# Performance work log

Measured on AMD Instinct MI355X. Metric: run time of the kernel, lower is better.

## Reference

```python
import jax, jax.numpy as jnp
import numpy as np

D_MODEL = 2048
N_HEADS = 16
D_HEAD = D_MODEL // N_HEADS  # 128
WINDOW = 512
SCALE = D_HEAD ** -0.5


def setup_inputs() -> dict:
    key = jax.random.key(0)
    ks = jax.random.split(key, 5)
    B, S = 2, 4096
    x = jax.random.normal(ks[0], (B, S, D_MODEL), dtype=jnp.float32)
    W_qkv = jax.random.normal(ks[1], (D_MODEL, 3 * D_MODEL), dtype=jnp.float32) * (D_MODEL ** -0.5)
    b_qkv = jax.random.normal(ks[2], (3 * D_MODEL,), dtype=jnp.float32) * 0.02
    W_out = jax.random.normal(ks[3], (D_MODEL, D_MODEL), dtype=jnp.float32) * (D_MODEL ** -0.5)
    b_out = jax.random.normal(ks[4], (D_MODEL,), dtype=jnp.float32) * 0.02
    return {"x": x, "W_qkv": W_qkv, "b_qkv": b_qkv, "W_out": W_out, "b_out": b_out}


def reference(x, W_qkv, b_qkv, W_out, b_out):
    B, S, D = x.shape
    nb = S // WINDOW  # number of independent causal windows (block-diagonal attention)
    qkv = x @ W_qkv + b_qkv  # (B,S,3D)
    q, k, v = jnp.split(qkv, 3, axis=-1)

    def to_blocks(t):
        # (B,S,D) -> (B,H,nb,W,dh)
        return t.reshape(B, nb, WINDOW, N_HEADS, D_HEAD).transpose(0, 3, 1, 2, 4)

    q, k, v = to_blocks(q), to_blocks(k), to_blocks(v)
    # per-window attention scores: (B,H,nb,W,W)
    scores = jnp.einsum('bhnqd,bhnkd->bhnqk', q, k) * SCALE
    causal = jnp.tril(jnp.ones((WINDOW, WINDOW), dtype=bool))
    scores = jnp.where(causal, scores, -jnp.inf)
    attn = jax.nn.softmax(scores, axis=-1)
    out = jnp.einsum('bhnqk,bhnkd->bhnqd', attn, v)  # (B,H,nb,W,dh)
    out = out.transpose(0, 2, 3, 1, 4).reshape(B, S, D)
    return out @ W_out + b_out
```

## Files before the change

### kernel.cpp

```cpp
#include <hip/hip_runtime.h>
#include <stdint.h>


typedef unsigned short u16;
typedef unsigned int u32;
typedef __attribute__((ext_vector_type(8))) short bf16x8;
typedef __attribute__((ext_vector_type(4))) float f32x4;

#define QKVN 6144
#define DM 2048

__device__ __forceinline__ u16 f2b(float f) {
  u32 u = __builtin_bit_cast(u32, f);
  u32 r = (u + 0x7fffu + ((u >> 16) & 1u)) >> 16;
  return (u16)r;
}

__device__ __forceinline__ void gload_lds16(const void* g, void* l) {
  __builtin_amdgcn_global_load_lds((const __attribute__((address_space(1))) void*)g,
                                   (__attribute__((address_space(3))) void*)l,
                                   16, 0, 0);
}


__global__ void cast_f32_bf16(const float4* __restrict__ x, uint4* __restrict__ o) {
  int idx = blockIdx.x * 256 + threadIdx.x;
  float4 a = x[2 * idx];
  float4 b = x[2 * idx + 1];
  uint4 r;
  r.x = (u32)f2b(a.x) | ((u32)f2b(a.y) << 16);
  r.y = (u32)f2b(a.z) | ((u32)f2b(a.w) << 16);
  r.z = (u32)f2b(b.x) | ((u32)f2b(b.y) << 16);
  r.w = (u32)f2b(b.z) | ((u32)f2b(b.w) << 16);
  o[idx] = r;
}

__global__ void transpose_cast(const float* __restrict__ W, u16* __restrict__ Wt,
                               int K, int N) {
  __shared__ u16 tile[64][65];
  int tx = threadIdx.x & 63;
  int ty = threadIdx.x >> 6;
  int n0 = blockIdx.x * 64;
  int k0 = blockIdx.y * 64;
#pragma unroll
  for (int r = 0; r < 64; r += 4)
    tile[r + ty][tx] = f2b(W[(size_t)(k0 + r + ty) * N + n0 + tx]);
  __syncthreads();
#pragma unroll
  for (int r = 0; r < 64; r += 4)
    Wt[(size_t)(n0 + r + ty) * K + k0 + tx] = tile[tx][r + ty];
}


template <typename TO>
__global__ __launch_bounds__(256, 3) void gemm_bt(const u16* __restrict__ A,
                                                  const u16* __restrict__ Bt,
                                                  const float* __restrict__ bias,
                                                  TO* __restrict__ C,
                                                  int M, int N, int K) {
  __shared__ u16 As[128 * 64];
  __shared__ u16 Bs[128 * 64];
  const int tid = threadIdx.x;
  const int lane = tid & 63;
  const int wave = tid >> 6;
  const int quad = lane >> 4;
  const int l15 = lane & 15;
  const int m0 = blockIdx.y * 128;
  const int n0 = blockIdx.x * 128;
  const int wm = (wave & 1) * 64;
  const int wn = (wave >> 1) * 64;

  f32x4 acc[4][4] = {};

  for (int k0 = 0; k0 < K; k0 += 64) {
#pragma unroll
    for (int i = 0; i < 4; ++i) {
      int sb = wave * 256 + i * 64;
      int s = sb + lane;
      int m = s >> 3;
      int c = (s & 7) ^ (m & 7);
      gload_lds16(A + (size_t)(m0 + m) * K + (k0 + c * 8), As + sb * 8);
      gload_lds16(Bt + (size_t)(n0 + m) * K + (k0 + c * 8), Bs + sb * 8);
    }
    __syncthreads();
#pragma unroll
    for (int ks = 0; ks < 2; ++ks) {
      bf16x8 af[4], bf[4];
#pragma unroll
      for (int i = 0; i < 4; ++i) {
        int m = wm + i * 16 + l15;
        af[i] = *(const bf16x8*)(As + m * 64 + (((ks * 4 + quad) ^ (m & 7)) << 3));
        int n = wn + i * 16 + l15;
        bf[i] = *(const bf16x8*)(Bs + n * 64 + (((ks * 4 + quad) ^ (n & 7)) << 3));
      }
#pragma unroll
      for (int i = 0; i < 4; ++i)
#pragma unroll
        for (int j = 0; j < 4; ++j)
          acc[i][j] = __builtin_amdgcn_mfma_f32_16x16x32_bf16(af[i], bf[j], acc[i][j], 0, 0, 0);
    }
    __syncthreads();
  }

#pragma unroll
  for (int j = 0; j < 4; ++j) {
    int col = n0 + wn + j * 16 + l15;
    float bv = bias[col];
#pragma unroll
    for (int i = 0; i < 4; ++i) {
      int row = m0 + wm + i * 16 + quad * 4;
#pragma unroll
      for (int t = 0; t < 4; ++t) {
        float v = acc[i][j][t] + bv;
        if constexpr (sizeof(TO) == 2)
          C[(size_t)(row + t) * N + col] = (TO)f2b(v);
        else
          C[(size_t)(row + t) * N + col] = (TO)v;
      }
    }
  }
}


__global__ __launch_bounds__(256, 2) void attn_win(const u16* __restrict__ qkv,
                                                   u16* __restrict__ attn_out) {
  __shared__ u16 Vt[128 * 64];
  __shared__ u16 Ps[128 * 64];
  const int tid = threadIdx.x;
  const int lane = tid & 63;
  const int wave = tid >> 6;
  const int quad = lane >> 4;
  const int l15 = lane & 15;
  const int qt = blockIdx.x;
  const int win = blockIdx.y;
  const int b = blockIdx.z >> 4;
  const int h = blockIdx.z & 15;
  const int tokw = b * 4096 + win * 512;
  const int tokq = tokw + qt * 128;
  const float SCALE = 0.08838834764831845f;

  bf16x8 qf[2][4];
  {
    const u16* Qb = qkv + (size_t)tokq * QKVN + h * 128;
#pragma unroll
    for (int j = 0; j < 2; ++j) {
      const u16* Qr = Qb + (size_t)(wave * 32 + j * 16 + l15) * QKVN + quad * 8;
#pragma unroll
      for (int ks = 0; ks < 4; ++ks)
        qf[j][ks] = *(const bf16x8*)(Qr + ks * 32);
    }
  }

  f32x4 acc_o[8][2] = {};
  float mrun[2] = {-1e30f, -1e30f};
  float lrun[2] = {0.f, 0.f};

  const int jt_end = 2 * qt + 1;
  for (int jt = 0; jt <= jt_end; ++jt) {
    {
      const u16* Vb = qkv + (size_t)(tokw + jt * 64) * QKVN + 4096 + h * 128;
#pragma unroll
      for (int it = 0; it < 2; ++it) {
        int task = it * 256 + tid;
        int p = task & 31;
        int dc = task >> 5;
        int kk0 = p * 2;
        const u16* g0 = Vb + (size_t)kk0 * QKVN + dc * 8;
        uint4 r0 = *(const uint4*)g0;
        uint4 r1 = *(const uint4*)(g0 + QKVN);
        const u16* a0 = (const u16*)&r0;
        const u16* a1 = (const u16*)&r1;
        int c = kk0 >> 3;
        int boff = (kk0 & 7) << 1;
#pragma unroll
        for (int j = 0; j < 8; ++j) {
          int d = dc * 8 + j;
          *(u32*)((char*)Vt + d * 128 + ((c ^ (d & 7)) << 4) + boff) =
              (u32)a0[j] | ((u32)a1[j] << 16);
        }
      }
    }

    f32x4 acc_s[4][2] = {};
    {
      const u16* Kb = qkv + (size_t)(tokw + jt * 64) * QKVN + 2048 + h * 128;
      bf16x8 kf[4][4];
#pragma unroll
      for (int i = 0; i < 4; ++i) {
        const u16* Kr = Kb + (size_t)(i * 16 + l15) * QKVN + quad * 8;
#pragma unroll
        for (int ks = 0; ks < 4; ++ks)
          kf[i][ks] = *(const bf16x8*)(Kr + ks * 32);
      }
#pragma unroll
      for (int ks = 0; ks < 4; ++ks)
#pragma unroll
        for (int i = 0; i < 4; ++i)
#pragma unroll
          for (int j = 0; j < 2; ++j)
            acc_s[i][j] = __builtin_amdgcn_mfma_f32_16x16x32_bf16(kf[i][ks], qf[j][ks],
                                                                  acc_s[i][j], 0, 0, 0);
    }

    const bool need_mask = (jt >= 2 * qt);
#pragma unroll
    for (int j = 0; j < 2; ++j) {
      int ql = wave * 32 + j * 16 + l15;
      int qg = qt * 128 + ql;
      float vmax = -1e30f;
#pragma unroll
      for (int i = 0; i < 4; ++i)
#pragma unroll
        for (int t = 0; t < 4; ++t) {
          float s = acc_s[i][j][t] * SCALE;
          if (need_mask) {
            int kg = jt * 64 + i * 16 + quad * 4 + t;
            if (kg > qg) s = -1e30f;
          }
          acc_s[i][j][t] = s;
          vmax = fmaxf(vmax, s);
        }
      vmax = fmaxf(vmax, __shfl_xor(vmax, 16));
      vmax = fmaxf(vmax, __shfl_xor(vmax, 32));
      float mnew = fmaxf(mrun[j], vmax);
      float alpha = __expf(mrun[j] - mnew);
      mrun[j] = mnew;
      float vsum = 0.f;
#pragma unroll
      for (int i = 0; i < 4; ++i) {
        float p0 = __expf(acc_s[i][j][0] - mnew);
        float p1 = __expf(acc_s[i][j][1] - mnew);
        float p2 = __expf(acc_s[i][j][2] - mnew);
        float p3 = __expf(acc_s[i][j][3] - mnew);
        vsum += (p0 + p1) + (p2 + p3);
        uint2 pk;
        pk.x = (u32)f2b(p0) | ((u32)f2b(p1) << 16);
        pk.y = (u32)f2b(p2) | ((u32)f2b(p3) << 16);
        int kk = i * 16 + quad * 4;
        *(uint2*)((char*)Ps + ql * 128 + (((kk >> 3) ^ (ql & 7)) << 4) + ((kk & 7) << 1)) = pk;
      }
      vsum += __shfl_xor(vsum, 16);
      vsum += __shfl_xor(vsum, 32);
      lrun[j] = lrun[j] * alpha + vsum;
#pragma unroll
      for (int i2 = 0; i2 < 8; ++i2)
#pragma unroll
        for (int t = 0; t < 4; ++t)
          acc_o[i2][j][t] *= alpha;
    }
    __syncthreads();

#pragma unroll
    for (int ks = 0; ks < 2; ++ks) {
      int kk = ks * 32 + quad * 8;
      int kc = kk >> 3;
      bf16x8 pf[2];
#pragma unroll
      for (int j = 0; j < 2; ++j) {
        int ql = wave * 32 + j * 16 + l15;
        pf[j] = *(const bf16x8*)((char*)Ps + ql * 128 + ((kc ^ (ql & 7)) << 4));
      }
#pragma unroll
      for (int i2 = 0; i2 < 8; ++i2) {
        int d = i2 * 16 + l15;
        bf16x8 vf = *(const bf16x8*)((char*)Vt + d * 128 + ((kc ^ (d & 7)) << 4));
#pragma unroll
        for (int j = 0; j < 2; ++j)
          acc_o[i2][j] = __builtin_amdgcn_mfma_f32_16x16x32_bf16(vf, pf[j], acc_o[i2][j], 0, 0, 0);
      }
    }
    __syncthreads();
  }

#pragma unroll
  for (int j = 0; j < 2; ++j) {
    float inv = 1.0f / lrun[j];
    int ql = wave * 32 + j * 16 + l15;
    u16* orow = attn_out + (size_t)(tokq + ql) * DM + h * 128;
#pragma unroll
    for (int i2 = 0; i2 < 8; ++i2) {
      int d = i2 * 16 + quad * 4;
      uint2 pk;
      pk.x = (u32)f2b(acc_o[i2][j][0] * inv) | ((u32)f2b(acc_o[i2][j][1] * inv) << 16);
      pk.y = (u32)f2b(acc_o[i2][j][2] * inv) | ((u32)f2b(acc_o[i2][j][3] * inv) << 16);
      *(uint2*)(orow + d) = pk;
    }
  }
}


extern "C" void kernel_launch(void* const* d_in, const int* in_sizes, int n_in,
                              void* d_out, int out_size, void* d_ws, size_t ws_size,
                              hipStream_t stream) {
  const float* x = (const float*)d_in[0];
  const float* W_qkv = (const float*)d_in[1];
  const float* b_qkv = (const float*)d_in[2];
  const float* W_out = (const float*)d_in[3];
  const float* b_out = (const float*)d_in[4];
  float* out = (float*)d_out;

  char* w = (char*)d_ws;
  u16* xb = (u16*)w;
  u16* wqkvT = (u16*)(w + 33554432);
  u16* woutT = (u16*)(w + 33554432 + 25165824);
  u16* qkv = (u16*)(w + 67108864);

  cast_f32_bf16<<<8192, 256, 0, stream>>>((const float4*)x, (uint4*)xb);
  transpose_cast<<<dim3(96, 32), 256, 0, stream>>>(W_qkv, wqkvT, 2048, 6144);
  transpose_cast<<<dim3(32, 32), 256, 0, stream>>>(W_out, woutT, 2048, 2048);
  gemm_bt<u16><<<dim3(48, 64), 256, 0, stream>>>(xb, wqkvT, b_qkv, qkv, 8192, 6144, 2048);
  attn_win<<<dim3(4, 8, 32), 256, 0, stream>>>(qkv, xb);
  gemm_bt<float><<<dim3(16, 64), 256, 0, stream>>>(xb, woutT, b_out, out, 8192, 2048, 2048);
}
```

Measured before the change: 522.3 us.

## Replace 128x128 GEMM with 256x256 multi-stage pipelined 8-wave GEMM

Both projection GEMMs now use a 256x256 tile with 8 waves and a 5/4-slot LDS ring buffer. The K loop is split into half-tile phases that interleave asynchronous global-to-LDS loads with MFMA bursts, using explicit waitcnt, barriers and setprio. A grid swizzle improves L2 reuse. It aims to raise arithmetic intensity and hide load latency, at the cost of heavy LDS use (72KB), more registers and fragile hand-tuned synchronization.

```diff
diff --git a/kernel.cpp b/kernel.cpp
--- a/kernel.cpp
+++ b/kernel.cpp
@@ -53,69 +53,167 @@
 
 
 template <typename TO>
-__global__ __launch_bounds__(256, 3) void gemm_bt(const u16* __restrict__ A,
-                                                  const u16* __restrict__ Bt,
-                                                  const float* __restrict__ bias,
-                                                  TO* __restrict__ C,
-                                                  int M, int N, int K) {
-  __shared__ u16 As[128 * 64];
-  __shared__ u16 Bs[128 * 64];
+__global__ __launch_bounds__(512, 2) void gemm_bt256(const u16* __restrict__ A,
+                                                     const u16* __restrict__ Bt,
+                                                     const float* __restrict__ bias,
+                                                     TO* __restrict__ C,
+                                                     int M, int N, int K, int nbx) {
+  __shared__ u16 As[5 * 8192];
+  __shared__ u16 Bs[4 * 8192];
   const int tid = threadIdx.x;
   const int lane = tid & 63;
   const int wave = tid >> 6;
+  const int wr = wave >> 2;
+  const int wc = wave & 3;
   const int quad = lane >> 4;
   const int l15 = lane & 15;
-  const int m0 = blockIdx.y * 128;
-  const int n0 = blockIdx.x * 128;
-  const int wm = (wave & 1) * 64;
-  const int wn = (wave >> 1) * 64;
-
-  f32x4 acc[4][4] = {};
-
-  for (int k0 = 0; k0 < K; k0 += 64) {
-#pragma unroll
-    for (int i = 0; i < 4; ++i) {
-      int sb = wave * 256 + i * 64;
-      int s = sb + lane;
-      int m = s >> 3;
-      int c = (s & 7) ^ (m & 7);
-      gload_lds16(A + (size_t)(m0 + m) * K + (k0 + c * 8), As + sb * 8);
-      gload_lds16(Bt + (size_t)(n0 + m) * K + (k0 + c * 8), Bs + sb * 8);
-    }
-    __syncthreads();
-#pragma unroll
-    for (int ks = 0; ks < 2; ++ks) {
-      bf16x8 af[4], bf[4];
-#pragma unroll
-      for (int i = 0; i < 4; ++i) {
-        int m = wm + i * 16 + l15;
-        af[i] = *(const bf16x8*)(As + m * 64 + (((ks * 4 + quad) ^ (m & 7)) << 3));
-        int n = wn + i * 16 + l15;
-        bf[i] = *(const bf16x8*)(Bs + n * 64 + (((ks * 4 + quad) ^ (n & 7)) << 3));
-      }
-#pragma unroll
-      for (int i = 0; i < 4; ++i)
-#pragma unroll
-        for (int j = 0; j < 4; ++j)
-          acc[i][j] = __builtin_amdgcn_mfma_f32_16x16x32_bf16(af[i], bf[j], acc[i][j], 0, 0, 0);
-    }
-    __syncthreads();
+
+  const int nwg = gridDim.x;
+  const int id = blockIdx.x;
+  const int swz = (id & 7) * (nwg >> 3) + (id >> 3);
+  const int bx = swz % nbx;
+  const int by = swz / nbx;
+  const int m0 = by * 256;
+  const int n0 = bx * 256;
+  const int NT = K >> 6;
+  const int NH = 2 * NT;
+
+  auto stageA = [&](int h, int slot) {
+    if (h < NH) {
+      const u16* src = A + (size_t)(m0 + ((h & 1) << 7)) * K + ((h >> 1) << 6);
+      u16* dst = As + slot * 8192 + (wave << 9);
+#pragma unroll
+      for (int it = 0; it < 2; ++it) {
+        int s = (it << 9) + (wave << 6) + lane;
+        int row = s >> 3;
+        int c = (s & 7) ^ (row & 7);
+        gload_lds16(src + (size_t)row * K + (c << 3), dst + (it << 12));
+      }
+    }
+  };
+  auto stageB = [&](int h, int slot) {
+    if (h < NH) {
+      const u16* src = Bt + (size_t)(n0 + ((h & 1) << 7)) * K + ((h >> 1) << 6);
+      u16* dst = Bs + slot * 8192 + (wave << 9);
+#pragma unroll
+      for (int it = 0; it < 2; ++it) {
+        int s = (it << 9) + (wave << 6) + lane;
+        int row = s >> 3;
+        int c = (s & 7) ^ (row & 7);
+        gload_lds16(src + (size_t)row * K + (c << 3), dst + (it << 12));
+      }
+    }
+  };
+
+  f32x4 acc[8][4] = {};
+  const int axq = l15 & 7;
+  const int aro = l15 << 6;
+  const int c0 = (quad ^ axq) << 3;
+  const int c1 = ((4 + quad) ^ axq) << 3;
+
+  stageA(0, 0); stageB(0, 0);
+  stageA(1, 1); stageB(1, 1);
+  stageA(2, 2); stageB(2, 2);
+  asm volatile("s_waitcnt vmcnt(4)" ::: "memory");
+  __builtin_amdgcn_s_barrier();
+
+  int sa = wr;
+  int h3a = 3;
+  int h4a = 4;
+
+  for (int t = 0; t < NT; ++t) {
+    const u16* ar = As + sa * 8192 + aro;
+    const u16* bp = Bs + (((2 * t + (wc >> 1)) & 3) * 8192) + ((wc & 1) << 12) + aro;
+    bf16x8 a0[4], a1[4], b0[4];
+
+#pragma unroll
+    for (int j = 0; j < 4; ++j) b0[j] = *(const bf16x8*)(bp + j * 1024 + c0);
+#pragma unroll
+    for (int i = 0; i < 4; ++i) a0[i] = *(const bf16x8*)(ar + i * 1024 + c0);
+    stageA(2 * t + 3, h3a);
+    __builtin_amdgcn_s_barrier();
+    asm volatile("s_waitcnt lgkmcnt(0)" ::: "memory");
+    __builtin_amdgcn_sched_barrier(0);
+    __builtin_amdgcn_s_setprio(1);
+#pragma unroll
+    for (int i = 0; i < 4; ++i)
+#pragma unroll
+      for (int j = 0; j < 4; ++j)
+        acc[i][j] = __builtin_amdgcn_mfma_f32_16x16x32_bf16(a0[i], b0[j], acc[i][j], 0, 0, 0);
+    __builtin_amdgcn_s_setprio(0);
+    __builtin_amdgcn_s_barrier();
+
+#pragma unroll
+    for (int i = 0; i < 4; ++i) a1[i] = *(const bf16x8*)(ar + (i + 4) * 1024 + c0);
+    stageB(2 * t + 3, (2 * t + 3) & 3);
+    __builtin_amdgcn_s_barrier();
+    asm volatile("s_waitcnt lgkmcnt(0)" ::: "memory");
+    __builtin_amdgcn_sched_barrier(0);
+    __builtin_amdgcn_s_setprio(1);
+#pragma unroll
+    for (int i = 0; i < 4; ++i)
+#pragma unroll
+      for (int j = 0; j < 4; ++j)
+        acc[i + 4][j] = __builtin_amdgcn_mfma_f32_16x16x32_bf16(a1[i], b0[j], acc[i + 4][j], 0, 0, 0);
+    __builtin_amdgcn_s_setprio(0);
+    __builtin_amdgcn_s_barrier();
+
+#pragma unroll
+    for (int j = 0; j < 4; ++j) b0[j] = *(const bf16x8*)(bp + j * 1024 + c1);
+#pragma unroll
+    for (int i = 0; i < 4; ++i) a0[i] = *(const bf16x8*)(ar + i * 1024 + c1);
+    stageA(2 * t + 4, h4a);
+    __builtin_amdgcn_s_barrier();
+    asm volatile("s_waitcnt lgkmcnt(0)" ::: "memory");
+    __builtin_amdgcn_sched_barrier(0);
+    __builtin_amdgcn_s_setprio(1);
+#pragma unroll
+    for (int i = 0; i < 4; ++i)
+#pragma unroll
+      for (int j = 0; j < 4; ++j)
+        acc[i][j] = __builtin_amdgcn_mfma_f32_16x16x32_bf16(a0[i], b0[j], acc[i][j], 0, 0, 0);
+    __builtin_amdgcn_s_setprio(0);
+    __builtin_amdgcn_s_barrier();
+
+#pragma unroll
+    for (int i = 0; i < 4; ++i) a1[i] = *(const bf16x8*)(ar + (i + 4) * 1024 + c1);
+    stageB(2 * t + 4, (2 * t + 4) & 3);
+    if (t + 3 <= NT) {
+      asm volatile("s_waitcnt vmcnt(4)" ::: "memory");
+    } else if (t + 2 == NT) {
+      asm volatile("s_waitcnt vmcnt(0)" ::: "memory");
+    }
+    __builtin_amdgcn_s_barrier();
+    asm volatile("s_waitcnt lgkmcnt(0)" ::: "memory");
+    __builtin_amdgcn_sched_barrier(0);
+    __builtin_amdgcn_s_setprio(1);
+#pragma unroll
+    for (int i = 0; i < 4; ++i)
+#pragma unroll
+      for (int j = 0; j < 4; ++j)
+        acc[i + 4][j] = __builtin_amdgcn_mfma_f32_16x16x32_bf16(a1[i], b0[j], acc[i + 4][j], 0, 0, 0);
+    __builtin_amdgcn_s_setprio(0);
+    __builtin_amdgcn_s_barrier();
+
+    sa += 2; if (sa >= 5) sa -= 5;
+    h3a += 2; if (h3a >= 5) h3a -= 5;
+    h4a += 2; if (h4a >= 5) h4a -= 5;
   }
 
 #pragma unroll
   for (int j = 0; j < 4; ++j) {
-    int col = n0 + wn + j * 16 + l15;
+    int col = n0 + wc * 64 + j * 16 + l15;
     float bv = bias[col];
 #pragma unroll
-    for (int i = 0; i < 4; ++i) {
-      int row = m0 + wm + i * 16 + quad * 4;
-#pragma unroll
-      for (int t = 0; t < 4; ++t) {
-        float v = acc[i][j][t] + bv;
+    for (int i = 0; i < 8; ++i) {
+      int row = m0 + wr * 128 + i * 16 + quad * 4;
+#pragma unroll
+      for (int tt = 0; tt < 4; ++tt) {
+        float v = acc[i][j][tt] + bv;
         if constexpr (sizeof(TO) == 2)
-          C[(size_t)(row + t) * N + col] = (TO)f2b(v);
+          C[(size_t)(row + tt) * N + col] = (TO)f2b(v);
         else
-          C[(size_t)(row + t) * N + col] = (TO)v;
+          C[(size_t)(row + tt) * N + col] = (TO)v;
       }
     }
   }
@@ -308,7 +406,7 @@
   cast_f32_bf16<<<8192, 256, 0, stream>>>((const float4*)x, (uint4*)xb);
   transpose_cast<<<dim3(96, 32), 256, 0, stream>>>(W_qkv, wqkvT, 2048, 6144);
   transpose_cast<<<dim3(32, 32), 256, 0, stream>>>(W_out, woutT, 2048, 2048);
-  gemm_bt<u16><<<dim3(48, 64), 256, 0, stream>>>(xb, wqkvT, b_qkv, qkv, 8192, 6144, 2048);
+  gemm_bt256<u16><<<768, 512, 0, stream>>>(xb, wqkvT, b_qkv, qkv, 8192, 6144, 2048, 24);
   attn_win<<<dim3(4, 8, 32), 256, 0, stream>>>(qkv, xb);
-  gemm_bt<float><<<dim3(16, 64), 256, 0, stream>>>(xb, woutT, b_out, out, 8192, 2048, 2048);
-}
+  gemm_bt256<float><<<256, 512, 0, stream>>>(xb, woutT, b_out, out, 8192, 2048, 2048, 8);
+}
```

After: 556.6 us. 6.6% more time.

## Emit V transposed from QKV GEMM and double-buffer V tiles via async LDS loads

Applied to the files above, without the earlier changes.

The QKV GEMM epilogue now writes the V columns in a transposed (d-major, token-contiguous) layout to a separate buffer, while Q and K go to a narrower 4096-wide buffer. The attention kernel then stages V tiles with direct global-to-LDS loads into a double buffer, prefetching the next tile while the current one is computed. This removes the per-iteration register transpose and scattered LDS writes. It also skips the accumulator rescale when the running max does not change. The cost is strided 8-byte stores in the GEMM epilogue for V and extra LDS use for the second buffer.

```diff
diff --git a/kernel.cpp b/kernel.cpp
--- a/kernel.cpp
+++ b/kernel.cpp
@@ -7,7 +7,7 @@
 typedef __attribute__((ext_vector_type(8))) short bf16x8;
 typedef __attribute__((ext_vector_type(4))) float f32x4;
 
-#define QKVN 6144
+#define QKN 4096
 #define DM 2048
 
 __device__ __forceinline__ u16 f2b(float f) {
@@ -57,7 +57,9 @@
                                                   const u16* __restrict__ Bt,
                                                   const float* __restrict__ bias,
                                                   TO* __restrict__ C,
-                                                  int M, int N, int K) {
+                                                  u16* __restrict__ vt,
+                                                  int M, int N, int K,
+                                                  int crstride, int vstart) {
   __shared__ u16 As[128 * 64];
   __shared__ u16 Bs[128 * 64];
   const int tid = threadIdx.x;
@@ -102,29 +104,47 @@
     __syncthreads();
   }
 
-#pragma unroll
-  for (int j = 0; j < 4; ++j) {
-    int col = n0 + wn + j * 16 + l15;
-    float bv = bias[col];
-#pragma unroll
-    for (int i = 0; i < 4; ++i) {
-      int row = m0 + wm + i * 16 + quad * 4;
-#pragma unroll
-      for (int t = 0; t < 4; ++t) {
-        float v = acc[i][j][t] + bv;
-        if constexpr (sizeof(TO) == 2)
-          C[(size_t)(row + t) * N + col] = (TO)f2b(v);
-        else
-          C[(size_t)(row + t) * N + col] = (TO)v;
-      }
-    }
-  }
-}
-
-
-__global__ __launch_bounds__(256, 2) void attn_win(const u16* __restrict__ qkv,
+  if (n0 >= vstart) {
+#pragma unroll
+    for (int j = 0; j < 4; ++j) {
+      int col = n0 + wn + j * 16 + l15;
+      float bv = bias[col];
+      u16* vcol = vt + (size_t)(col - vstart) * 8192;
+#pragma unroll
+      for (int i = 0; i < 4; ++i) {
+        int row = m0 + wm + i * 16 + quad * 4;
+        uint2 pk;
+        pk.x = (u32)f2b(acc[i][j][0] + bv) | ((u32)f2b(acc[i][j][1] + bv) << 16);
+        pk.y = (u32)f2b(acc[i][j][2] + bv) | ((u32)f2b(acc[i][j][3] + bv) << 16);
+        *(uint2*)(vcol + row) = pk;
+      }
+    }
+  } else {
+#pragma unroll
+    for (int j = 0; j < 4; ++j) {
+      int col = n0 + wn + j * 16 + l15;
+      float bv = bias[col];
+#pragma unroll
+      for (int i = 0; i < 4; ++i) {
+        int row = m0 + wm + i * 16 + quad * 4;
+#pragma unroll
+        for (int t = 0; t < 4; ++t) {
+          float v = acc[i][j][t] + bv;
+          if constexpr (sizeof(TO) == 2)
+            C[(size_t)(row + t) * crstride + col] = (TO)f2b(v);
+          else
+            C[(size_t)(row + t) * crstride + col] = (TO)v;
+        }
+      }
+    }
+  }
+}
+
+
+__global__ __launch_bounds__(256, 2) void attn_win(const u16* __restrict__ qk,
+                                                   const u16* __restrict__ vt,
                                                    u16* __restrict__ attn_out) {
-  __shared__ u16 Vt[128 * 64];
+  __shared__ u16 Vs[2][8192];
   __shared__ u16 Ps[128 * 64];
   const int tid = threadIdx.x;
   const int lane = tid & 63;
@@ -139,12 +159,26 @@
   const int tokq = tokw + qt * 128;
   const float SCALE = 0.08838834764831845f;
 
+  auto stageV = [&](int jt, int buf) {
+    const u16* vbase = vt + (size_t)(h * 128) * 8192 + (tokw + jt * 64);
+    char* dst0 = (char*)Vs[buf] + wave * 1024;
+#pragma unroll
+    for (int it = 0; it < 4; ++it) {
+      int ch = it * 256 + wave * 64 + lane;
+      int row = ch >> 3;
+      int c = (ch & 7) ^ (row & 7);
+      gload_lds16(vbase + (size_t)row * 8192 + c * 8, dst0 + it * 4096);
+    }
+  };
+
+  stageV(0, 0);
+
   bf16x8 qf[2][4];
   {
-    const u16* Qb = qkv + (size_t)tokq * QKVN + h * 128;
+    const u16* Qb = qk + (size_t)tokq * QKN + h * 128;
 #pragma unroll
     for (int j = 0; j < 2; ++j) {
-      const u16* Qr = Qb + (size_t)(wave * 32 + j * 16 + l15) * QKVN + quad * 8;
+      const u16* Qr = Qb + (size_t)(wave * 32 + j * 16 + l15) * QKN + quad * 8;
 #pragma unroll
       for (int ks = 0; ks < 4; ++ks)
         qf[j][ks] = *(const bf16x8*)(Qr + ks * 32);
@@ -157,37 +191,15 @@
 
   const int jt_end = 2 * qt + 1;
   for (int jt = 0; jt <= jt_end; ++jt) {
-    {
-      const u16* Vb = qkv + (size_t)(tokw + jt * 64) * QKVN + 4096 + h * 128;
-#pragma unroll
-      for (int it = 0; it < 2; ++it) {
-        int task = it * 256 + tid;
-        int p = task & 31;
-        int dc = task >> 5;
-        int kk0 = p * 2;
-        const u16* g0 = Vb + (size_t)kk0 * QKVN + dc * 8;
-        uint4 r0 = *(const uint4*)g0;
-        uint4 r1 = *(const uint4*)(g0 + QKVN);
-        const u16* a0 = (const u16*)&r0;
-        const u16* a1 = (const u16*)&r1;
-        int c = kk0 >> 3;
-        int boff = (kk0 & 7) << 1;
-#pragma unroll
-        for (int j = 0; j < 8; ++j) {
-          int d = dc * 8 + j;
-          *(u32*)((char*)Vt + d * 128 + ((c ^ (d & 7)) << 4) + boff) =
-              (u32)a0[j] | ((u32)a1[j] << 16);
-        }
-      }
-    }
+    if (jt < jt_end) stageV(jt + 1, (jt + 1) & 1);
 
     f32x4 acc_s[4][2] = {};
     {
-      const u16* Kb = qkv + (size_t)(tokw + jt * 64) * QKVN + 2048 + h * 128;
+      const u16* Kb = qk + (size_t)(tokw + jt * 64) * QKN + 2048 + h * 128;
       bf16x8 kf[4][4];
 #pragma unroll
       for (int i = 0; i < 4; ++i) {
-        const u16* Kr = Kb + (size_t)(i * 16 + l15) * QKVN + quad * 8;
+        const u16* Kr = Kb + (size_t)(i * 16 + l15) * QKN + quad * 8;
 #pragma unroll
         for (int ks = 0; ks < 4; ++ks)
           kf[i][ks] = *(const bf16x8*)(Kr + ks * 32);
@@ -222,9 +234,17 @@
         }
       vmax = fmaxf(vmax, __shfl_xor(vmax, 16));
       vmax = fmaxf(vmax, __shfl_xor(vmax, 32));
-      float mnew = fmaxf(mrun[j], vmax);
-      float alpha = __expf(mrun[j] - mnew);
-      mrun[j] = mnew;
+      if (vmax > mrun[j]) {
+        float alpha = __expf(mrun[j] - vmax);
+        mrun[j] = vmax;
+        lrun[j] *= alpha;
+#pragma unroll
+        for (int i2 = 0; i2 < 8; ++i2)
+#pragma unroll
+          for (int t = 0; t < 4; ++t)
+            acc_o[i2][j][t] *= alpha;
+      }
+      float mnew = mrun[j];
       float vsum = 0.f;
 #pragma unroll
       for (int i = 0; i < 4; ++i) {
@@ -241,15 +261,11 @@
       }
       vsum += __shfl_xor(vsum, 16);
       vsum += __shfl_xor(vsum, 32);
-      lrun[j] = lrun[j] * alpha + vsum;
-#pragma unroll
-      for (int i2 = 0; i2 < 8; ++i2)
-#pragma unroll
-        for (int t = 0; t < 4; ++t)
-          acc_o[i2][j][t] *= alpha;
+      lrun[j] += vsum;
     }
     __syncthreads();
 
+    const u16* Vtile = Vs[jt & 1];
 #pragma unroll
     for (int ks = 0; ks < 2; ++ks) {
       int kk = ks * 32 + quad * 8;
@@ -263,7 +279,7 @@
 #pragma unroll
       for (int i2 = 0; i2 < 8; ++i2) {
         int d = i2 * 16 + l15;
-        bf16x8 vf = *(const bf16x8*)((char*)Vt + d * 128 + ((kc ^ (d & 7)) << 4));
+        bf16x8 vf = *(const bf16x8*)((char*)Vtile + d * 128 + ((kc ^ (d & 7)) << 4));
 #pragma unroll
         for (int j = 0; j < 2; ++j)
           acc_o[i2][j] = __builtin_amdgcn_mfma_f32_16x16x32_bf16(vf, pf[j], acc_o[i2][j], 0, 0, 0);
@@ -301,14 +317,17 @@
 
   char* w = (char*)d_ws;
   u16* xb = (u16*)w;
-  u16* wqkvT = (u16*)(w + 33554432);
-  u16* woutT = (u16*)(w + 33554432 + 25165824);
-  u16* qkv = (u16*)(w + 67108864);
+  u16* wqkvT = (u16*)(w + (32u << 20));
+  u16* woutT = (u16*)(w + (56u << 20));
+  u16* qk = (u16*)(w + (64u << 20));
+  u16* vtb = (u16*)(w + (128u << 20));
 
   cast_f32_bf16<<<8192, 256, 0, stream>>>((const float4*)x, (uint4*)xb);
   transpose_cast<<<dim3(96, 32), 256, 0, stream>>>(W_qkv, wqkvT, 2048, 6144);
   transpose_cast<<<dim3(32, 32), 256, 0, stream>>>(W_out, woutT, 2048, 2048);
-  gemm_bt<u16><<<dim3(48, 64), 256, 0, stream>>>(xb, wqkvT, b_qkv, qkv, 8192, 6144, 2048);
-  attn_win<<<dim3(4, 8, 32), 256, 0, stream>>>(qkv, xb);
-  gemm_bt<float><<<dim3(16, 64), 256, 0, stream>>>(xb, woutT, b_out, out, 8192, 2048, 2048);
-}
+  gemm_bt<u16><<<dim3(48, 64), 256, 0, stream>>>(xb, wqkvT, b_qkv, qk, vtb,
+                                                 8192, 6144, 2048, 4096, 4096);
+  attn_win<<<dim3(4, 8, 32), 256, 0, stream>>>(qk, vtb, xb);
+  gemm_bt<float><<<dim3(16, 64), 256, 0, stream>>>(xb, woutT, b_out, out, vtb,
+                                                   8192, 2048, 2048, 2048, 1 << 28);
+}
```

New measurement: 511.8 us. -2.0%, faster.
